# Performance work log

Measured on AMD Instinct MI355X. Metric: run time of the kernel, lower is better.

## Reference

```python
import jax, jax.numpy as jnp
import numpy as np

N_NODES = 100000
N_EDGES = 1600000
IN_DIM, HID_DIM, OUT_DIM = 256, 128, 128


def gcn_norm(edge_index, edge_weight, num_nodes):
    # Add self-loops with weight 1 (PyG GCNConv default fill_value=1.0)
    loop = jnp.arange(num_nodes, dtype=edge_index.dtype)
    src = jnp.concatenate([edge_index[0], loop])
    dst = jnp.concatenate([edge_index[1], loop])
    w = jnp.concatenate([edge_weight, jnp.ones((num_nodes,), edge_weight.dtype)])
    # Symmetric normalization: deg computed at destination over edge weights
    deg = jax.ops.segment_sum(w, dst, num_segments=num_nodes)
    dinv = jnp.where(deg > 0, jax.lax.rsqrt(deg), 0.0)
    norm = dinv[src] * w * dinv[dst]  # [E + N]
    return src, dst, norm


def gcn_conv(x, W, b, src, dst, norm, num_nodes):
    h = x @ W                                  # [N, out]
    msg = h[src] * norm[:, None]               # gather + scale, [E+N, out]
    out = jax.ops.segment_sum(msg, dst, num_segments=num_nodes)  # scatter-add
    return out + b


def setup_inputs() -> dict:
    key = jax.random.key(0)
    ks = jax.random.split(key, 8)
    x = jax.random.normal(ks[0], (N_NODES, IN_DIM), dtype=jnp.float32)
    edge_index = jax.random.randint(ks[1], (2, N_EDGES), 0, N_NODES, dtype=jnp.int64)
    edge_weight = jax.random.uniform(ks[2], (N_EDGES,), dtype=jnp.float32)
    s1 = 1.0 / np.sqrt(IN_DIM)
    s2 = 1.0 / np.sqrt(HID_DIM)
    W1 = jax.random.uniform(ks[3], (IN_DIM, HID_DIM), jnp.float32, -s1, s1)
    b1 = jnp.zeros((HID_DIM,), jnp.float32)
    W2 = jax.random.uniform(ks[4], (HID_DIM, OUT_DIM), jnp.float32, -s2, s2)
    b2 = jnp.zeros((OUT_DIM,), jnp.float32)
    return {"x": x, "edge_index": edge_index, "edge_weight": edge_weight,
            "W1": W1, "b1": b1, "W2": W2, "b2": b2}


def reference(x, edge_index, edge_weight, W1, b1, W2, b2):
    n = x.shape[0]
    src, dst, norm = gcn_norm(edge_index, edge_weight, n)
    h = jax.nn.relu(gcn_conv(x, W1, b1, src, dst, norm, n))
    out = gcn_conv(h, W2, b2, src, dst, norm, n)
    return out
```

## Files before the change

kernel.cpp:

```cpp
#include <hip/hip_runtime.h>
#include <stdint.h>

#define N_NODES 100000
#define N_EDGES 1600000
#define IN_DIM 256
#define HID_DIM 128
#define OUT_DIM 128

#define NBUCK 391
#define CHUNK 4096

typedef __attribute__((ext_vector_type(8))) short short8;
typedef __attribute__((ext_vector_type(4))) float floatx4;

__device__ __forceinline__ float bf2f(unsigned short u) {
    union { unsigned int i; float f; } v; v.i = ((unsigned int)u) << 16; return v.f;
}
__device__ __forceinline__ unsigned short f2bf(float f) {
    union { float fl; unsigned int i; } v; v.fl = f;
    unsigned int x = v.i;
    return (unsigned short)((x + 0x7fffu + ((x >> 16) & 1u)) >> 16);
}
__device__ __forceinline__ float bflo(unsigned int u) {
    union { unsigned int i; float f; } v; v.i = u << 16; return v.f;
}
__device__ __forceinline__ float bfhi(unsigned int u) {
    union { unsigned int i; float f; } v; v.i = u & 0xffff0000u; return v.f;
}
__device__ __forceinline__ float asf(unsigned int u) {
    union { unsigned int i; float f; } v; v.i = u; return v.f;
}
__device__ __forceinline__ unsigned int asu(float f) {
    union { float fl; unsigned int i; } v; v.fl = f; return v.i;
}
__device__ __forceinline__ unsigned int pack2(float a, float b) {
    unsigned int ua = asu(a), ub = asu(b);
    ua += 0x7fffu + ((ua >> 16) & 1u);
    ub += 0x7fffu + ((ub >> 16) & 1u);
    return (ua >> 16) | (ub & 0xffff0000u);
}
__device__ __forceinline__ short8 pack8(float4 a, float4 b) {
    union { unsigned int u[4]; short8 s; } r;
    r.u[0] = pack2(a.x, a.y);
    r.u[1] = pack2(a.z, a.w);
    r.u[2] = pack2(b.x, b.y);
    r.u[3] = pack2(b.z, b.w);
    return r.s;
}

__global__ void k_detect(const unsigned int* __restrict__ xu, const unsigned int* __restrict__ eu,
                         int* __restrict__ flags, int* __restrict__ bucket_cnt) {
    __shared__ int s_huge, s_odd;
    if (threadIdx.x == 0) { s_huge = 0; s_odd = 0; }
    if (threadIdx.x < NBUCK) bucket_cnt[threadIdx.x] = 0;
    __syncthreads();
    int huge = 0, odd = 0;
    for (int i = threadIdx.x; i < 1024; i += 512) {
        unsigned int b = xu[i];
        unsigned int e = (b >> 23) & 0xffu;
        if (e >= 0xf0u) huge = 1;
        if (eu[2 * i + 1] != 0) odd = 1;
    }
    if (huge) atomicOr(&s_huge, 1);
    if (odd) atomicOr(&s_odd, 1);
    __syncthreads();
    if (threadIdx.x == 0) { flags[0] = s_huge ? 0 : 1; flags[1] = s_odd ? 0 : 1; }
}

__device__ __forceinline__ int load_idx(const void* base, long long i, int i64m) {
    int v = i64m ? (int)((const long long*)base)[i] : ((const int*)base)[i];
    return v < 0 ? 0 : (v >= N_NODES ? N_NODES - 1 : v);
}
__device__ __forceinline__ float load_f(const void* base, long long i, int f32m) {
    return f32m ? ((const float*)base)[i] : bf2f(((const unsigned short*)base)[i]);
}

__global__ void k_bhist(const void* __restrict__ ei, const int* __restrict__ flags,
                        int* __restrict__ bucket_cnt, float* __restrict__ wdeg, int e) {
    __shared__ int h[NBUCK];
    for (int t = threadIdx.x; t < NBUCK; t += 256) h[t] = 0;
    int z = blockIdx.x * 256 + threadIdx.x;
    if (z < N_NODES) wdeg[z] = 0.f;
    __syncthreads();
    int i64m = flags[1];
    int base = blockIdx.x * CHUNK;
    int end = base + CHUNK < e ? base + CHUNK : e;
    for (int i = base + threadIdx.x; i < end; i += 256) {
        int d = load_idx(ei, (long long)N_EDGES + i, i64m);
        atomicAdd(&h[d >> 8], 1);
    }
    __syncthreads();
    for (int t = threadIdx.x; t < NBUCK; t += 256)
        if (h[t]) atomicAdd(&bucket_cnt[t], h[t]);
}

__global__ void k_bscan(const int* __restrict__ bucket_cnt, int* __restrict__ bucket_base,
                        int* __restrict__ bucket_cursor, int* __restrict__ rowptr) {
    __shared__ int lds[512];
    int t = threadIdx.x;
    int v = (t < NBUCK) ? bucket_cnt[t] : 0;
    lds[t] = v;
    __syncthreads();
    for (int off = 1; off < 512; off <<= 1) {
        int x = (t >= off) ? lds[t - off] : 0;
        __syncthreads();
        lds[t] += x;
        __syncthreads();
    }
    int excl = lds[t] - v;
    if (t < NBUCK) { bucket_base[t] = excl; bucket_cursor[t] = excl; }
    if (t == 0) { bucket_base[NBUCK] = lds[NBUCK - 1]; rowptr[N_NODES] = N_EDGES; }
}

__global__ void k_bscatter(const void* __restrict__ ei, const void* __restrict__ ew,
                           const int* __restrict__ flags, int* __restrict__ bucket_cursor,
                           uint2* __restrict__ ebuf, float* __restrict__ wdeg, int e) {
    __shared__ int h[NBUCK];
    for (int t = threadIdx.x; t < NBUCK; t += 256) h[t] = 0;
    __syncthreads();
    int f32m = flags[0], i64m = flags[1];
    int base = blockIdx.x * CHUNK;
    int end = base + CHUNK < e ? base + CHUNK : e;
    for (int i = base + threadIdx.x; i < end; i += 256) {
        int d = load_idx(ei, (long long)N_EDGES + i, i64m);
        atomicAdd(&h[d >> 8], 1);
    }
    __syncthreads();
    for (int t = threadIdx.x; t < NBUCK; t += 256) {
        int c = h[t];
        h[t] = c ? atomicAdd(&bucket_cursor[t], c) : 0;
    }
    __syncthreads();
    for (int i = base + threadIdx.x; i < end; i += 256) {
        int s = load_idx(ei, i, i64m);
        int d = load_idx(ei, (long long)N_EDGES + i, i64m);
        float w = load_f(ew, i, f32m);
        atomicAdd(&wdeg[d], w);
        int b = d >> 8;
        int p = atomicAdd(&h[b], 1);
        uint2 c; c.x = (unsigned int)s | ((unsigned int)(d & 255) << 17); c.y = asu(w);
        ebuf[p] = c;
    }
}

__global__ void k_dinv(const float* __restrict__ wdeg, float* __restrict__ dinv, int n) {
    int i = blockIdx.x * 256 + threadIdx.x;
    if (i < n) dinv[i] = rsqrtf(1.0f + wdeg[i]);
}

__global__ void k_fine(const uint2* __restrict__ ebuf, const int* __restrict__ bucket_base,
                       const float* __restrict__ dinv, uint2* __restrict__ csr,
                       int* __restrict__ rowptr, int n) {
    __shared__ int h[256];
    __shared__ int c2[256];
    int t = threadIdx.x, b = blockIdx.x;
    int e0 = bucket_base[b], e1 = bucket_base[b + 1];
    h[t] = 0;
    __syncthreads();
    for (int i = e0 + t; i < e1; i += 256) {
        uint2 c = ebuf[i];
        int dl = (c.x >> 17) & 255;
        atomicAdd(&h[dl], 1);
    }
    __syncthreads();
    int own = h[t];
    for (int off = 1; off < 256; off <<= 1) {
        int x = (t >= off) ? h[t - off] : 0;
        __syncthreads();
        h[t] += x;
        __syncthreads();
    }
    int excl = h[t] - own;
    int node = (b << 8) + t;
    if (node < n) rowptr[node] = e0 + excl;
    c2[t] = e0 + excl;
    __syncthreads();
    for (int i = e0 + t; i < e1; i += 256) {
        uint2 c = ebuf[i];
        int dl = (c.x >> 17) & 255;
        int p = atomicAdd(&c2[dl], 1);
        c.y = asu(asf(c.y) * dinv[c.x & 0x1FFFF]);
        csr[p] = c;
    }
}

__global__ void k_transpose(const void* __restrict__ W1, const void* __restrict__ W2,
                            const int* __restrict__ flags,
                            unsigned short* __restrict__ W1T, unsigned short* __restrict__ W2T) {
    int i = blockIdx.x * 256 + threadIdx.x;
    int f32m = flags[0];
    if (i < IN_DIM * HID_DIM) {
        int k = i / HID_DIM, n = i % HID_DIM;
        W1T[n * IN_DIM + k] = f2bf(load_f(W1, i, f32m));
    } else {
        int j = i - IN_DIM * HID_DIM;
        if (j < HID_DIM * OUT_DIM) {
            int k = j / OUT_DIM, n = j % OUT_DIM;
            W2T[n * HID_DIM + k] = f2bf(load_f(W2, j, f32m));
        }
    }
}

template <int KH, bool F32M>
__device__ __forceinline__ void gemm_loop(const void* __restrict__ A,
                                          const unsigned short* __restrict__ Bs,
                                          size_t aoff0, size_t aoff1,
                                          int quad, int l16, floatx4 (&acc)[2][8]) {
    constexpr int NCH = KH / 32;
    constexpr int BMASK = KH / 8 - 1;
    float4 fraw[2][2];
    short8 braw[2];
    if (F32M) {
        const float* ap = (const float*)A;
        fraw[0][0] = *(const float4*)(ap + aoff0);
        fraw[0][1] = *(const float4*)(ap + aoff0 + 4);
        fraw[1][0] = *(const float4*)(ap + aoff1);
        fraw[1][1] = *(const float4*)(ap + aoff1 + 4);
    } else {
        const unsigned short* ap = (const unsigned short*)A;
        braw[0] = *(const short8*)(ap + aoff0);
        braw[1] = *(const short8*)(ap + aoff1);
    }
#pragma unroll
    for (int ch = 0; ch < NCH; ch++) {
        float4 nf[2][2];
        short8 nb[2];
        if (ch + 1 < NCH) {
            int o = (ch + 1) * 32;
            if (F32M) {
                const float* ap = (const float*)A;
                nf[0][0] = *(const float4*)(ap + aoff0 + o);
                nf[0][1] = *(const float4*)(ap + aoff0 + o + 4);
                nf[1][0] = *(const float4*)(ap + aoff1 + o);
                nf[1][1] = *(const float4*)(ap + aoff1 + o + 4);
            } else {
                const unsigned short* ap = (const unsigned short*)A;
                nb[0] = *(const short8*)(ap + aoff0 + o);
                nb[1] = *(const short8*)(ap + aoff1 + o);
            }
        }
        short8 a0, a1;
        if (F32M) {
            a0 = pack8(fraw[0][0], fraw[0][1]);
            a1 = pack8(fraw[1][0], fraw[1][1]);
        } else {
            a0 = braw[0];
            a1 = braw[1];
        }
#pragma unroll
        for (int c = 0; c < 8; c++) {
            int col = c * 16 + l16;
            int boff = col * KH + 8 * ((ch * 4 + quad + (col & 7)) & BMASK);
            short8 bf = *(const short8*)(Bs + boff);
            acc[0][c] = __builtin_amdgcn_mfma_f32_16x16x32_bf16(a0, bf, acc[0][c], 0, 0, 0);
            acc[1][c] = __builtin_amdgcn_mfma_f32_16x16x32_bf16(a1, bf, acc[1][c], 0, 0, 0);
        }
        if (ch + 1 < NCH) {
            if (F32M) {
                fraw[0][0] = nf[0][0]; fraw[0][1] = nf[0][1];
                fraw[1][0] = nf[1][0]; fraw[1][1] = nf[1][1];
            } else {
                braw[0] = nb[0]; braw[1] = nb[1];
            }
        }
    }
}

template <int K, bool RAWA>
__global__ void k_gemm(const void* __restrict__ A, const unsigned short* __restrict__ WT,
                       unsigned short* __restrict__ H, const int* __restrict__ flags, int n) {
    constexpr int KH = (K > 128) ? 128 : K;
    __shared__ unsigned short Bs[128 * KH];

    int wave = threadIdx.x >> 6;
    int lane = threadIdx.x & 63;
    int quad = lane >> 4;
    int l16 = lane & 15;
    int rowbase = blockIdx.x * 128 + wave * 32;
    int r0 = rowbase + l16;        if (r0 >= n) r0 = n - 1;
    int r1 = rowbase + 16 + l16;   if (r1 >= n) r1 = n - 1;
    size_t aoff0 = (size_t)r0 * K + quad * 8;
    size_t aoff1 = (size_t)r1 * K + quad * 8;

    floatx4 acc[2][8];
#pragma unroll
    for (int t = 0; t < 2; t++)
#pragma unroll
        for (int c = 0; c < 8; c++) acc[t][c] = (floatx4){0.f, 0.f, 0.f, 0.f};

    int f32m = RAWA ? flags[0] : 0;

#pragma unroll
    for (int hh = 0; hh < K / KH; hh++) {
        if (hh) __syncthreads();
        for (int base = threadIdx.x * 8; base < 128 * KH; base += 256 * 8) {
            int col = base / KH;
            int k = base - col * KH;
            int ks = (k + (col & 7) * 8) & (KH - 1);
            *(short8*)(&Bs[col * KH + ks]) = *(const short8*)(WT + col * K + hh * KH + k);
        }
        __syncthreads();
        if (RAWA && f32m)
            gemm_loop<KH, true>(A, Bs, aoff0 + hh * KH, aoff1 + hh * KH, quad, l16, acc);
        else
            gemm_loop<KH, false>(A, Bs, aoff0 + hh * KH, aoff1 + hh * KH, quad, l16, acc);
    }

#pragma unroll
    for (int t = 0; t < 2; t++)
#pragma unroll
        for (int c = 0; c < 8; c++)
#pragma unroll
            for (int r = 0; r < 4; r++) {
                int grow = rowbase + t * 16 + quad * 4 + r;
                if (grow < n) H[(size_t)grow * 128 + c * 16 + l16] = f2bf(acc[t][c][r]);
            }
}

__device__ __forceinline__ void acc8(float wt, uint4 hv, float* a) {
    a[0] += wt * bflo(hv.x); a[1] += wt * bfhi(hv.x);
    a[2] += wt * bflo(hv.y); a[3] += wt * bfhi(hv.y);
    a[4] += wt * bflo(hv.z); a[5] += wt * bfhi(hv.z);
    a[6] += wt * bflo(hv.w); a[7] += wt * bfhi(hv.w);
}

template <bool RELU, bool FINAL>
__global__ void k_aggregate(const unsigned short* __restrict__ H, const int* __restrict__ rowptr,
                            const uint2* __restrict__ csr, const float* __restrict__ dinv,
                            const void* __restrict__ bias, void* __restrict__ out,
                            const int* __restrict__ flags, int n) {
    int node = blockIdx.x * 16 + (threadIdx.x >> 4);
    int lane = threadIdx.x & 15;
    if (node >= n) return;
    int col = lane * 8;
    int f32m = flags[0];

    int e0 = rowptr[node], e1 = rowptr[node + 1];
    uint4 u = *(const uint4*)(H + (size_t)node * 128 + col);
    float dn = dinv[node];

    float a[8] = {0.f, 0.f, 0.f, 0.f, 0.f, 0.f, 0.f, 0.f};

    const uint2* ep = csr + e0;
    int nb = (e1 - e0) >> 2;
    uint2 c0, c1, c2, c3;
    uint4 h0, h1, h2, h3;
    if (nb) {
        c0 = ep[0]; c1 = ep[1]; c2 = ep[2]; c3 = ep[3];
        h0 = *(const uint4*)(H + (size_t)(c0.x & 0x1FFFF) * 128 + col);
        h1 = *(const uint4*)(H + (size_t)(c1.x & 0x1FFFF) * 128 + col);
        h2 = *(const uint4*)(H + (size_t)(c2.x & 0x1FFFF) * 128 + col);
        h3 = *(const uint4*)(H + (size_t)(c3.x & 0x1FFFF) * 128 + col);
    }
    for (int b = 1; b < nb; b++) {
        const uint2* np = ep + 4 * b;
        uint2 d0 = np[0], d1 = np[1], d2 = np[2], d3 = np[3];
        uint4 g0 = *(const uint4*)(H + (size_t)(d0.x & 0x1FFFF) * 128 + col);
        uint4 g1 = *(const uint4*)(H + (size_t)(d1.x & 0x1FFFF) * 128 + col);
        uint4 g2 = *(const uint4*)(H + (size_t)(d2.x & 0x1FFFF) * 128 + col);
        uint4 g3 = *(const uint4*)(H + (size_t)(d3.x & 0x1FFFF) * 128 + col);
        acc8(asf(c0.y), h0, a); acc8(asf(c1.y), h1, a);
        acc8(asf(c2.y), h2, a); acc8(asf(c3.y), h3, a);
        c0 = d0; c1 = d1; c2 = d2; c3 = d3;
        h0 = g0; h1 = g1; h2 = g2; h3 = g3;
    }
    if (nb) {
        acc8(asf(c0.y), h0, a); acc8(asf(c1.y), h1, a);
        acc8(asf(c2.y), h2, a); acc8(asf(c3.y), h3, a);
    }
    for (int e = e0 + (nb << 2); e < e1; e++) {
        uint2 c = csr[e];
        uint4 hh = *(const uint4*)(H + (size_t)(c.x & 0x1FFFF) * 128 + col);
        acc8(asf(c.y), hh, a);
    }

    float coef = dn * dn;
    a[0] = dn * a[0] + coef * bflo(u.x) + load_f(bias, col, f32m);
    a[1] = dn * a[1] + coef * bfhi(u.x) + load_f(bias, col + 1, f32m);
    a[2] = dn * a[2] + coef * bflo(u.y) + load_f(bias, col + 2, f32m);
    a[3] = dn * a[3] + coef * bfhi(u.y) + load_f(bias, col + 3, f32m);
    a[4] = dn * a[4] + coef * bflo(u.z) + load_f(bias, col + 4, f32m);
    a[5] = dn * a[5] + coef * bfhi(u.z) + load_f(bias, col + 5, f32m);
    a[6] = dn * a[6] + coef * bflo(u.w) + load_f(bias, col + 6, f32m);
    a[7] = dn * a[7] + coef * bfhi(u.w) + load_f(bias, col + 7, f32m);

    if (RELU) {
#pragma unroll
        for (int i = 0; i < 8; i++) a[i] = fmaxf(a[i], 0.f);
    }
    if (FINAL && f32m) {
        float* op = (float*)out + (size_t)node * 128 + col;
        float4 o0 = {a[0], a[1], a[2], a[3]};
        float4 o1 = {a[4], a[5], a[6], a[7]};
        *(float4*)op = o0;
        *(float4*)(op + 4) = o1;
    } else {
        uint4 o;
        o.x = pack2(a[0], a[1]); o.y = pack2(a[2], a[3]);
        o.z = pack2(a[4], a[5]); o.w = pack2(a[6], a[7]);
        *(uint4*)((unsigned short*)out + (size_t)node * 128 + col) = o;
    }
}

extern "C" void kernel_launch(void* const* d_in, const int* in_sizes, int n_in,
                              void* d_out, int out_size, void* d_ws, size_t ws_size,
                              hipStream_t stream) {
    const void* x  = d_in[0];
    const void* ei = d_in[1];
    const void* ew = d_in[2];
    const void* W1 = d_in[3];
    const void* b1 = d_in[4];
    const void* W2 = d_in[5];
    const void* b2 = d_in[6];

    char* p = (char*)d_ws;
    auto alloc = [&](size_t bytes) { char* r = p; p += (bytes + 255) & ~(size_t)255; return r; };
    int*   flags    = (int*)alloc(256);
    float* dinv     = (float*)alloc((size_t)N_NODES * 4);
    float* wdeg     = (float*)alloc((size_t)N_NODES * 4);
    int*   rowptr   = (int*)alloc((size_t)(N_NODES + 1) * 4);
    int*   bucket_cnt    = (int*)alloc((size_t)NBUCK * 4);
    int*   bucket_base   = (int*)alloc((size_t)(NBUCK + 1) * 4);
    int*   bucket_cursor = (int*)alloc((size_t)NBUCK * 4);
    uint2* csr      = (uint2*)alloc((size_t)N_EDGES * 8);
    unsigned short* W1T  = (unsigned short*)alloc((size_t)IN_DIM * HID_DIM * 2);
    unsigned short* W2T  = (unsigned short*)alloc((size_t)HID_DIM * OUT_DIM * 2);
    unsigned short* hbuf = (unsigned short*)alloc((size_t)N_NODES * 128 * 2);
    unsigned short* zbuf = (unsigned short*)alloc((size_t)N_NODES * 128 * 2);
    uint2* ebuf = (uint2*)hbuf;

    int nbC = (N_EDGES + CHUNK - 1) / CHUNK;
    int nbN = (N_NODES + 255) / 256;
    int nbG = (N_NODES + 127) / 128;
    int nbA = (N_NODES + 15) / 16;

    k_detect<<<1, 512, 0, stream>>>((const unsigned int*)x, (const unsigned int*)ei, flags, bucket_cnt);
    k_bhist<<<nbC, 256, 0, stream>>>(ei, flags, bucket_cnt, wdeg, N_EDGES);
    k_bscan<<<1, 512, 0, stream>>>(bucket_cnt, bucket_base, bucket_cursor, rowptr);
    k_bscatter<<<nbC, 256, 0, stream>>>(ei, ew, flags, bucket_cursor, ebuf, wdeg, N_EDGES);
    k_dinv<<<nbN, 256, 0, stream>>>(wdeg, dinv, N_NODES);
    k_fine<<<NBUCK, 256, 0, stream>>>(ebuf, bucket_base, dinv, csr, rowptr, N_NODES);
    k_transpose<<<(IN_DIM * HID_DIM + HID_DIM * OUT_DIM + 255) / 256, 256, 0, stream>>>(W1, W2, flags, W1T, W2T);

    k_gemm<IN_DIM, true><<<nbG, 256, 0, stream>>>(x, W1T, hbuf, flags, N_NODES);
    k_aggregate<true, false><<<nbA, 256, 0, stream>>>(hbuf, rowptr, csr, dinv,
                                                      b1, zbuf, flags, N_NODES);
    k_gemm<HID_DIM, false><<<nbG, 256, 0, stream>>>(zbuf, W2T, hbuf, flags, N_NODES);
    k_aggregate<false, true><<<nbA, 256, 0, stream>>>(hbuf, rowptr, csr, dinv,
                                                      b2, d_out, flags, N_NODES);
}
```

Before: 513.0 us.

## Compute weighted degree in LDS during bucket sort, fold source dinv separately

Removes the global float atomicAdd into wdeg from the scatter kernel and drops the separate dinv kernel. Each fine-sort block now sums edge weights per destination in shared memory and writes dinv directly. Since dinv for source nodes is not ready inside k_fine, a new k_fold pass rescales each CSR weight by dinv[src], two edges per thread. This trades 1.6M global atomics for an extra read-modify-write pass over the 12.8MB CSR array.

```diff
diff --git a/kernel.cpp b/kernel.cpp
--- a/kernel.cpp
+++ b/kernel.cpp
@@ -76,11 +76,9 @@
 }
 
 __global__ void k_bhist(const void* __restrict__ ei, const int* __restrict__ flags,
-                        int* __restrict__ bucket_cnt, float* __restrict__ wdeg, int e) {
+                        int* __restrict__ bucket_cnt, int e) {
     __shared__ int h[NBUCK];
     for (int t = threadIdx.x; t < NBUCK; t += 256) h[t] = 0;
-    int z = blockIdx.x * 256 + threadIdx.x;
-    if (z < N_NODES) wdeg[z] = 0.f;
     __syncthreads();
     int i64m = flags[1];
     int base = blockIdx.x * CHUNK;
@@ -114,7 +112,7 @@
 
 __global__ void k_bscatter(const void* __restrict__ ei, const void* __restrict__ ew,
                            const int* __restrict__ flags, int* __restrict__ bucket_cursor,
-                           uint2* __restrict__ ebuf, float* __restrict__ wdeg, int e) {
+                           uint2* __restrict__ ebuf, int e) {
     __shared__ int h[NBUCK];
     for (int t = threadIdx.x; t < NBUCK; t += 256) h[t] = 0;
     __syncthreads();
@@ -135,7 +133,6 @@
         int s = load_idx(ei, i, i64m);
         int d = load_idx(ei, (long long)N_EDGES + i, i64m);
         float w = load_f(ew, i, f32m);
-        atomicAdd(&wdeg[d], w);
         int b = d >> 8;
         int p = atomicAdd(&h[b], 1);
         uint2 c; c.x = (unsigned int)s | ((unsigned int)(d & 255) << 17); c.y = asu(w);
@@ -143,24 +140,21 @@
     }
 }
 
-__global__ void k_dinv(const float* __restrict__ wdeg, float* __restrict__ dinv, int n) {
-    int i = blockIdx.x * 256 + threadIdx.x;
-    if (i < n) dinv[i] = rsqrtf(1.0f + wdeg[i]);
-}
-
 __global__ void k_fine(const uint2* __restrict__ ebuf, const int* __restrict__ bucket_base,
-                       const float* __restrict__ dinv, uint2* __restrict__ csr,
-                       int* __restrict__ rowptr, int n) {
+                       uint2* __restrict__ csr, int* __restrict__ rowptr,
+                       float* __restrict__ dinv, int n) {
     __shared__ int h[256];
+    __shared__ float fw[256];
     __shared__ int c2[256];
     int t = threadIdx.x, b = blockIdx.x;
     int e0 = bucket_base[b], e1 = bucket_base[b + 1];
-    h[t] = 0;
+    h[t] = 0; fw[t] = 0.f;
     __syncthreads();
     for (int i = e0 + t; i < e1; i += 256) {
         uint2 c = ebuf[i];
         int dl = (c.x >> 17) & 255;
         atomicAdd(&h[dl], 1);
+        atomicAdd(&fw[dl], asf(c.y));
     }
     __syncthreads();
     int own = h[t];
@@ -172,16 +166,27 @@
     }
     int excl = h[t] - own;
     int node = (b << 8) + t;
-    if (node < n) rowptr[node] = e0 + excl;
+    if (node < n) {
+        rowptr[node] = e0 + excl;
+        dinv[node] = rsqrtf(1.0f + fw[t]);
+    }
     c2[t] = e0 + excl;
     __syncthreads();
     for (int i = e0 + t; i < e1; i += 256) {
         uint2 c = ebuf[i];
         int dl = (c.x >> 17) & 255;
         int p = atomicAdd(&c2[dl], 1);
-        c.y = asu(asf(c.y) * dinv[c.x & 0x1FFFF]);
         csr[p] = c;
     }
+}
+
+__global__ void k_fold(uint4* __restrict__ csr4, const float* __restrict__ dinv, int npair) {
+    int i = blockIdx.x * 256 + threadIdx.x;
+    if (i >= npair) return;
+    uint4 c = csr4[i];
+    c.y = asu(asf(c.y) * dinv[c.x & 0x1FFFF]);
+    c.w = asu(asf(c.w) * dinv[c.z & 0x1FFFF]);
+    csr4[i] = c;
 }
 
 __global__ void k_transpose(const void* __restrict__ W1, const void* __restrict__ W2,
@@ -417,7 +422,6 @@
     auto alloc = [&](size_t bytes) { char* r = p; p += (bytes + 255) & ~(size_t)255; return r; };
     int*   flags    = (int*)alloc(256);
     float* dinv     = (float*)alloc((size_t)N_NODES * 4);
-    float* wdeg     = (float*)alloc((size_t)N_NODES * 4);
     int*   rowptr   = (int*)alloc((size_t)(N_NODES + 1) * 4);
     int*   bucket_cnt    = (int*)alloc((size_t)NBUCK * 4);
     int*   bucket_base   = (int*)alloc((size_t)(NBUCK + 1) * 4);
@@ -430,16 +434,16 @@
     uint2* ebuf = (uint2*)hbuf;
 
     int nbC = (N_EDGES + CHUNK - 1) / CHUNK;
-    int nbN = (N_NODES + 255) / 256;
     int nbG = (N_NODES + 127) / 128;
     int nbA = (N_NODES + 15) / 16;
+    int nbF = (N_EDGES / 2 + 255) / 256;
 
     k_detect<<<1, 512, 0, stream>>>((const unsigned int*)x, (const unsigned int*)ei, flags, bucket_cnt);
-    k_bhist<<<nbC, 256, 0, stream>>>(ei, flags, bucket_cnt, wdeg, N_EDGES);
+    k_bhist<<<nbC, 256, 0, stream>>>(ei, flags, bucket_cnt, N_EDGES);
     k_bscan<<<1, 512, 0, stream>>>(bucket_cnt, bucket_base, bucket_cursor, rowptr);
-    k_bscatter<<<nbC, 256, 0, stream>>>(ei, ew, flags, bucket_cursor, ebuf, wdeg, N_EDGES);
-    k_dinv<<<nbN, 256, 0, stream>>>(wdeg, dinv, N_NODES);
-    k_fine<<<NBUCK, 256, 0, stream>>>(ebuf, bucket_base, dinv, csr, rowptr, N_NODES);
+    k_bscatter<<<nbC, 256, 0, stream>>>(ei, ew, flags, bucket_cursor, ebuf, N_EDGES);
+    k_fine<<<NBUCK, 256, 0, stream>>>(ebuf, bucket_base, csr, rowptr, dinv, N_NODES);
+    k_fold<<<nbF, 256, 0, stream>>>((uint4*)csr, dinv, N_EDGES / 2);
     k_transpose<<<(IN_DIM * HID_DIM + HID_DIM * OUT_DIM + 255) / 256, 256, 0, stream>>>(W1, W2, flags, W1T, W2T);
 
     k_gemm<IN_DIM, true><<<nbG, 256, 0, stream>>>(x, W1T, hbuf, flags, N_NODES);
```

Result: faster. 465.7 us (-9.2%).
